# Optimization experiments

Hardware: AMD Instinct MI355X
Metric: run time of the kernel (lower is better)

Reference implementation:

```python
import jax, jax.numpy as jnp
import numpy as np

N = 50000   # nodes
E = 400000  # edges (before self-loops)
F = 128     # num_features
H = 8       # heads (layer 1)
C = 64      # hidden_channels
B = 64      # graphs in batch
K = 10      # num_classes
NEG_SLOPE = 0.2


def setup_inputs() -> dict:
    key = jax.random.key(0)
    ks = jax.random.split(key, 12)
    g = lambda k, shape, fan: jax.random.normal(k, shape, jnp.float32) / np.sqrt(fan).astype(np.float32)
    return {
        "x": jax.random.normal(ks[0], (N, F), jnp.float32),
        "edge_index": jax.random.randint(ks[1], (2, E), 0, N, jnp.int32),
        "batch": jnp.sort(jax.random.randint(ks[2], (N,), 0, B, jnp.int32)),
        "W1": g(ks[3], (F, H * C), F),
        "att_src1": g(ks[4], (H, C), C),
        "att_dst1": g(ks[5], (H, C), C),
        "b1": jnp.zeros((H * C,), jnp.float32),
        "W2": g(ks[6], (H * C, C), H * C),
        "att_src2": g(ks[7], (1, C), C),
        "att_dst2": g(ks[8], (1, C), C),
        "b2": jnp.zeros((C,), jnp.float32),
        "lin1_w": g(ks[9], (C, C), C),
        "lin1_b": jnp.zeros((C,), jnp.float32),
        "lin2_w": g(ks[10], (C, K), C),
        "lin2_b": jnp.zeros((K,), jnp.float32),
    }


def gat_conv(x, src, dst, W, att_src, att_dst, bias):
    """PyG GATConv (self-loops already appended to src/dst). x:[N,Fin] -> [N,H*C]."""
    heads, out_c = att_src.shape
    h = (x @ W).reshape(N, heads, out_c)                      # [N,H,C]
    a_s = jnp.einsum('nhc,hc->nh', h, att_src)                # [N,H]
    a_d = jnp.einsum('nhc,hc->nh', h, att_dst)
    e = jax.nn.leaky_relu(a_s[src] + a_d[dst], NEG_SLOPE)     # [E',H]
    # segment softmax over incoming edges of each destination node
    m = jax.ops.segment_max(e, dst, num_segments=N)
    e = jnp.exp(e - m[dst])
    denom = jax.ops.segment_sum(e, dst, num_segments=N)
    alpha = e / (denom[dst] + 1e-16)                          # [E',H]
    out = jax.ops.segment_sum(h[src] * alpha[:, :, None], dst, num_segments=N)  # [N,H,C]
    return out.reshape(N, heads * out_c) + bias


def reference(x, edge_index, batch, W1, att_src1, att_dst1, b1,
              W2, att_src2, att_dst2, b2, lin1_w, lin1_b, lin2_w, lin2_b):
    loops = jnp.arange(N, dtype=edge_index.dtype)
    src = jnp.concatenate([edge_index[0], loops])
    dst = jnp.concatenate([edge_index[1], loops])

    h = gat_conv(x, src, dst, W1, att_src1, att_dst1, b1)     # [N, H*C]
    h = jax.nn.elu(h)                                         # dropout inactive (eval)
    h = gat_conv(h, src, dst, W2, att_src2, att_dst2, b2)     # [N, C]
    h = jax.nn.elu(h)

    pooled = jax.ops.segment_sum(h, batch, num_segments=B)    # global_add_pool -> [B, C]
    z = jax.nn.elu(pooled @ lin1_w + lin1_b)
    logits = z @ lin2_w + lin2_b
    return jax.nn.log_softmax(logits, axis=-1)
```

## Files before the change

kernel.cpp:

```cpp
#include <hip/hip_runtime.h>
#include <hip/hip_bf16.h>

#define DEV static __device__ __forceinline__

constexpr int F1 = 128;
constexpr int H1 = 8;
constexpr int C  = 64;
constexpr int B  = 64;
constexpr int K  = 10;
constexpr float NEG = 0.2f;
constexpr unsigned SMASK = 0x07FFFFFFu;

typedef __attribute__((ext_vector_type(8))) short short8;
typedef __attribute__((ext_vector_type(4))) float floatx4;

DEV float b2f(__hip_bfloat16 x) { return __bfloat162float(x); }
DEV float elu1(float v) { return v > 0.f ? v : (__expf(v) - 1.f); }
DEV unsigned short f2bbits(float f) {
  __hip_bfloat16 b = __float2bfloat16(f);
  return *(unsigned short*)&b;
}
DEV float blo(unsigned u) { return __uint_as_float(u << 16); }
DEV float bhi(unsigned u) { return __uint_as_float(u & 0xffff0000u); }
DEV float bu(unsigned short u) { return __uint_as_float(((unsigned)u) << 16); }
DEV unsigned pack2(float lo, float hi) {
  return (unsigned)f2bbits(lo) | ((unsigned)f2bbits(hi) << 16);
}
DEV float rcp_nr(float x) {
  float r = __builtin_amdgcn_rcpf(x);
  return r * (2.f - x * r);
}


DEV int detect_dev(const void* xraw, int* lds) {
  if (threadIdx.x == 0) {
    const __hip_bfloat16* xb = (const __hip_bfloat16*)xraw;
    int bad = 0;
    for (int i = 0; i < 128; ++i) {
      float v = b2f(xb[2 * i]);
      if (!(fabsf(v) < 1e4f)) bad++;
    }
    *lds = (bad < 13) ? 1 : 0;
  }
  __syncthreads();
  return *lds;
}

#define CVT(p, i) (isbf ? b2f(((const __hip_bfloat16*)(p))[i]) : ((const float*)(p))[i])

__global__ void fused_prep_kernel(const void* x_raw, const void* w1raw,
                                  const void* as1r, const void* ad1r, const void* b1r,
                                  const void* w2raw,
                                  const void* as2r, const void* ad2r, const void* b2r,
                                  const void* l1wr, const void* l1br,
                                  const void* l2wr, const void* l2br,
                                  unsigned short* __restrict__ xbf,
                                  unsigned short* __restrict__ w1frag,
                                  unsigned short* __restrict__ w2frag,
                                  unsigned short* __restrict__ vfrag,
                                  float* __restrict__ wts,
                                  int* __restrict__ deg,
                                  float* __restrict__ pooled,
                                  int nX, int N) {
  __shared__ int fl;
  int isbf = detect_dev(x_raw, &fl);
  int gid = blockIdx.x * 256 + threadIdx.x;
  int stride = gridDim.x * 256;

  if (isbf) {
    const unsigned short* src = (const unsigned short*)x_raw;
    for (int i = gid; i < nX; i += stride) xbf[i] = src[i];
  } else {
    const float* src = (const float*)x_raw;
    for (int i = gid; i < nX; i += stride) xbf[i] = f2bbits(src[i]);
  }
  for (int i = gid; i < 512;  i += stride) {
    int hp = i >> 7, l16 = (i >> 3) & 15, nt = i & 7;
    int c = hp * 128 + nt * 16 + l16;
    wts[1024 + i] = CVT(b1r, c);
  }
  for (int i = gid; i < 64;   i += stride) wts[1536 + i] = CVT(as2r, i);
  for (int i = gid; i < 64;   i += stride) wts[1600 + i] = CVT(ad2r, i);
  for (int i = gid; i < 64;   i += stride) wts[1664 + i] = CVT(b2r, i);
  for (int i = gid; i < 4096; i += stride) wts[1728 + i] = CVT(l1wr, i);
  for (int i = gid; i < 64;   i += stride) wts[5824 + i] = CVT(l1br, i);
  for (int i = gid; i < 640;  i += stride) wts[5888 + i] = CVT(l2wr, i);
  for (int i = gid; i < 10;   i += stride) wts[6528 + i] = CVT(l2br, i);
  for (int t = gid; t < 8192; t += stride) {
    int lane = t & 63, ks = (t >> 6) & 3, nt = t >> 8;
    for (int j = 0; j < 8; ++j) {
      int k = ks * 32 + (lane >> 4) * 8 + j;
      int n = nt * 16 + (lane & 15);
      w1frag[t * 8 + j] = f2bbits(CVT(w1raw, k * 512 + n));
    }
  }
  for (int t = gid; t < 4096; t += stride) {
    int lane = t & 63, nt = (t >> 6) & 3, ks = t >> 8;
    for (int j = 0; j < 8; ++j) {
      int p = ks * 32 + (lane >> 4) * 8 + j;
      int hp = p >> 7, pl16 = (p >> 3) & 15, pnt = p & 7;
      int k = hp * 128 + pnt * 16 + pl16;
      int n = nt * 16 + (lane & 15);
      w2frag[t * 8 + j] = f2bbits(CVT(w2raw, k * 64 + n));
    }
  }
  for (int t = gid; t < 2048; t += stride) {
    int j = t & 7, lane = (t >> 3) & 63, ks = t >> 9;
    int k = ks * 32 + (lane >> 4) * 8 + j;
    int n = lane & 15;
    int hh = (n < 8) ? n : (n - 8);
    float s = 0.f;
    if (n < 8) {
      for (int c = 0; c < 64; ++c)
        s += CVT(w1raw, k * 512 + hh * 64 + c) * CVT(as1r, hh * 64 + c);
    } else {
      for (int c = 0; c < 64; ++c)
        s += CVT(w1raw, k * 512 + hh * 64 + c) * CVT(ad1r, hh * 64 + c);
    }
    vfrag[(ks * 64 + lane) * 8 + j] = f2bbits(s);
  }
  for (int i = gid; i < N; i += stride) deg[i] = 0;
  for (int i = gid; i < B * C; i += stride) pooled[i] = 0.f;
}

__global__ void deg_count_kernel(const int* __restrict__ ei, int E, int Etot,
                                 int* __restrict__ deg) {
  int e = blockIdx.x * blockDim.x + threadIdx.x;
  if (e >= Etot) return;
  int d = (e < E) ? ei[E + e] : e - E;
  atomicAdd(&deg[d], 1);
}

__global__ void scan_block_kernel(const int* __restrict__ deg,
                                  int* __restrict__ local,
                                  int* __restrict__ bsum, int N) {
  __shared__ int tmp[256];
  int t = threadIdx.x;
  int i = blockIdx.x * 256 + t;
  int v = (i < N) ? deg[i] : 0;
  tmp[t] = v;
  __syncthreads();
  for (int off = 1; off < 256; off <<= 1) {
    int u = (t >= off) ? tmp[t - off] : 0;
    __syncthreads();
    tmp[t] += u;
    __syncthreads();
  }
  if (i < N) local[i] = tmp[t] - v;
  if (t == 255) bsum[blockIdx.x] = tmp[255];
}

__global__ void scan_finish_kernel(const int* __restrict__ local,
                                   const int* __restrict__ bsum, int nb,
                                   int* __restrict__ rowptr,
                                   int* __restrict__ cursor, int N, int Etot) {
  __shared__ int tmp[256];
  __shared__ int offs;
  int t = threadIdx.x;
  int v0 = (t < nb) ? bsum[t] : 0;
  tmp[t] = v0;
  __syncthreads();
  for (int off = 1; off < 256; off <<= 1) {
    int u = (t >= off) ? tmp[t - off] : 0;
    __syncthreads();
    tmp[t] += u;
    __syncthreads();
  }
  if (t == (int)blockIdx.x) offs = tmp[t] - v0;
  __syncthreads();
  int i = blockIdx.x * 256 + t;
  if (i < N) {
    int r = local[i] + offs;
    rowptr[i] = r;
    cursor[i] = r;
  }
  if (i == 0) rowptr[N] = Etot;
}

__global__ __launch_bounds__(256) void att_scalars_kernel(
    const unsigned short* __restrict__ xbf,
    const unsigned short* __restrict__ vfrag,
    float* __restrict__ a_s, float* __restrict__ a_d,
    int N) {
  int t = threadIdx.x, w = t >> 6, lane = t & 63;
  int quad = lane >> 4, l16 = lane & 15;
  int row0 = blockIdx.x * 64 + w * 16;

  floatx4 acc = {};
  int rl = row0 + l16; if (rl >= N) rl = N - 1;
  const unsigned short* xp = xbf + (size_t)rl * 128 + quad * 8;
#pragma unroll
  for (int ks = 0; ks < 4; ++ks) {
    short8 a = *(const short8*)(xp + ks * 32);
    short8 b = *(const short8*)&vfrag[(ks * 64 + lane) * 8];
    acc = __builtin_amdgcn_mfma_f32_16x16x32_bf16(a, b, acc, 0, 0, 0);
  }
#pragma unroll
  for (int r = 0; r < 4; ++r) {
    int row = row0 + quad * 4 + r;
    if (row < N) {
      if (l16 < 8) a_s[(size_t)row * 8 + l16] = acc[r];
      else         a_d[(size_t)row * 8 + (l16 - 8)] = acc[r];
    }
  }
}

__global__ void fill_weight_kernel(const int* __restrict__ ei, int E, int Etot,
                                   const float* __restrict__ a_s,
                                   const float* __restrict__ a_d,
                                   int* __restrict__ cursor,
                                   int* __restrict__ col,
                                   unsigned short* __restrict__ wedge) {
  int e = blockIdx.x * 256 + threadIdx.x;
  if (e >= Etot) return;
  int s, d;
  if (e < E) { s = ei[e]; d = ei[E + e]; } else { s = d = e - E; }
  int pos = atomicAdd(&cursor[d], 1);
  col[pos] = s | ((d & 15) << 27);
  float4 s0 = *(const float4*)(a_s + (size_t)s * 8);
  float4 s1 = *(const float4*)(a_s + (size_t)s * 8 + 4);
  float4 d0 = *(const float4*)(a_d + (size_t)d * 8);
  float4 d1 = *(const float4*)(a_d + (size_t)d * 8 + 4);
  float v, w0, w1, w2, w3, w4, w5, w6, w7;
  v = s0.x + d0.x; v = v > 0.f ? v : NEG * v; w0 = __expf(v);
  v = s0.y + d0.y; v = v > 0.f ? v : NEG * v; w1 = __expf(v);
  v = s0.z + d0.z; v = v > 0.f ? v : NEG * v; w2 = __expf(v);
  v = s0.w + d0.w; v = v > 0.f ? v : NEG * v; w3 = __expf(v);
  v = s1.x + d1.x; v = v > 0.f ? v : NEG * v; w4 = __expf(v);
  v = s1.y + d1.y; v = v > 0.f ? v : NEG * v; w5 = __expf(v);
  v = s1.z + d1.z; v = v > 0.f ? v : NEG * v; w6 = __expf(v);
  v = s1.w + d1.w; v = v > 0.f ? v : NEG * v; w7 = __expf(v);
  uint4 o;
  o.x = pack2(w0, w1); o.y = pack2(w2, w3);
  o.z = pack2(w4, w5); o.w = pack2(w6, w7);
  *(uint4*)(wedge + (size_t)pos * 8) = o;
}

__global__ __launch_bounds__(512, 6) void aggx_gemm1_kernel(
    const unsigned short* __restrict__ xbf,
    const unsigned short* __restrict__ W1frag,
    const int* __restrict__ rowptr,
    const int* __restrict__ col,
    const unsigned short* __restrict__ wedge,
    const float* __restrict__ bias_perm,
    unsigned short* __restrict__ out1,
    int N) {
  __shared__ __align__(16) char LB[8 * 16 * 136 * 2];
  unsigned short* XgT = (unsigned short*)LB;
  unsigned short* Wm  = (unsigned short*)(LB + 8192);
  unsigned short* AggP = (unsigned short*)LB;

  int t = threadIdx.x, w = t >> 6, lane = t & 63;
  int q = lane >> 4, n = lane & 15;
  int dbase = blockIdx.x * 16;

  int R0 = rowptr[dbase];
  int R1 = rowptr[min(dbase + 16, N)];
  int nch = (R1 - R0 + 31) >> 5;

  int kp = t >> 5, pp = t & 31;
  int skey = ((pp >> 1) & 7) << 4;
  int dw = t >> 5, kw = t & 31;

  short8 onesf = {};
  if (n == 0) {
#pragma unroll
    for (int j = 0; j < 8; ++j) onesf[j] = (short)0x3F80;
  }

  floatx4 accw[8] = {};
  floatx4 accdn = {};

  for (int c = 0; c < nch; ++c) {
    int ebase = R0 + c * 32;
    __syncthreads();

    {
      int e0 = ebase + 2 * kp;
      int ec0 = (e0 < R1) ? e0 : (R1 - 1);
      int ec1 = (e0 + 1 < R1) ? (e0 + 1) : (R1 - 1);
      int s0 = col[ec0] & SMASK;
      int s1 = col[ec1] & SMASK;
      uint2 xa = *(const uint2*)(xbf + (size_t)s0 * 128 + pp * 4);
      uint2 xb = *(const uint2*)(xbf + (size_t)s1 * 128 + pp * 4);
      int base = 256 * pp + 4 * kp;
      unsigned w0 = (xa.x & 0xffffu) | (xb.x << 16);
      unsigned w1 = (xa.x >> 16) | (xb.x & 0xffff0000u);
      unsigned w2 = (xa.y & 0xffffu) | (xb.y << 16);
      unsigned w3 = (xa.y >> 16) | (xb.y & 0xffff0000u);
      *(unsigned*)((char*)XgT + ((base)       ^ skey)) = w0;
      *(unsigned*)((char*)XgT + ((base + 64)  ^ skey)) = w1;
      *(unsigned*)((char*)XgT + ((base + 128) ^ skey)) = w2;
      *(unsigned*)((char*)XgT + ((base + 192) ^ skey)) = w3;
    }
    {
      int ew = ebase + kw;
      bool evw = ew < R1;
      int ewc = evw ? ew : (R1 - 1);
      int cv = col[ewc];
      int dl = (cv >> 27) & 15;
      uint4 wv = *(const uint4*)(wedge + (size_t)ewc * 8);
      bool mine = evw && (dl == dw);
      unsigned short* wmp = Wm + dw * 32 + kw;
      wmp[0]    = mine ? (unsigned short)(wv.x & 0xffff) : 0;
      wmp[512]  = mine ? (unsigned short)(wv.x >> 16)    : 0;
      wmp[1024] = mine ? (unsigned short)(wv.y & 0xffff) : 0;
      wmp[1536] = mine ? (unsigned short)(wv.y >> 16)    : 0;
      wmp[2048] = mine ? (unsigned short)(wv.z & 0xffff) : 0;
      wmp[2560] = mine ? (unsigned short)(wv.z >> 16)    : 0;
      wmp[3072] = mine ? (unsigned short)(wv.w & 0xffff) : 0;
      wmp[3584] = mine ? (unsigned short)(wv.w >> 16)    : 0;
    }
    __syncthreads();

    short8 af = *(const short8*)(Wm + w * 512 + n * 32 + 8 * q);
    accdn = __builtin_amdgcn_mfma_f32_16x16x32_bf16(af, onesf, accdn, 0, 0, 0);
#pragma unroll
    for (int ft = 0; ft < 8; ++ft) {
      int bb = (ft * 16 + n) * 64 + 16 * q;
      bb ^= ((bb >> 9) & 7) << 4;
      short8 bfr = *(const short8*)((const char*)XgT + bb);
      accw[ft] = __builtin_amdgcn_mfma_f32_16x16x32_bf16(af, bfr, accw[ft], 0, 0, 0);
    }
  }

  __syncthreads();

  {
    float dnv[4];
#pragma unroll
    for (int r = 0; r < 4; ++r) {
      float dr = __shfl(accdn[r], lane & 48);
      dnv[r] = rcp_nr(dr + 1e-16f);
    }
#pragma unroll
    for (int ft = 0; ft < 8; ++ft)
#pragma unroll
      for (int r = 0; r < 4; ++r)
        AggP[w * 2176 + (4 * q + r) * 136 + ft * 16 + n] =
            f2bbits(accw[ft][r] * dnv[r]);
  }
  __syncthreads();

  {
    int hp = w >> 1, qq = w & 1;
    floatx4 acc2[4] = {};
    const unsigned short* Bp = W1frag + (size_t)hp * 16384;
#pragma unroll
    for (int ks = 0; ks < 4; ++ks) {
      short8 a2 = *(const short8*)&AggP[w * 2176 + n * 136 + ks * 32 + q * 8];
#pragma unroll
      for (int j = 0; j < 4; ++j) {
        int nt = qq * 4 + j;
        short8 b2 = *(const short8*)&Bp[((nt * 4 + ks) * 64 + lane) * 8];
        acc2[j] = __builtin_amdgcn_mfma_f32_16x16x32_bf16(a2, b2, acc2[j], 0, 0, 0);
      }
    }
    float4 bq = *(const float4*)&bias_perm[hp * 128 + n * 8 + qq * 4];
#pragma unroll
    for (int r = 0; r < 4; ++r) {
      int row = dbase + 4 * q + r;
      if (row < N) {
        uint2 o;
        o.x = pack2(elu1(acc2[0][r] + bq.x), elu1(acc2[1][r] + bq.y));
        o.y = pack2(elu1(acc2[2][r] + bq.z), elu1(acc2[3][r] + bq.w));
        *(uint2*)&out1[(size_t)row * 512 + hp * 128 + n * 8 + qq * 4] = o;
      }
    }
  }
}

__global__ __launch_bounds__(256) void gemm2_mfma_kernel(
    const unsigned short* __restrict__ x2bf,
    const unsigned short* __restrict__ W2frag,
    const float* __restrict__ att_src,
    const float* __restrict__ att_dst,
    unsigned short* __restrict__ h2,
    float* __restrict__ a_s, float* __restrict__ a_d,
    int N) {
  int t = threadIdx.x;
  int w = t >> 6, lane = t & 63;
  int quad = lane >> 4, l16 = lane & 15;
  int rowbase = blockIdx.x * 64 + w * 16;

  floatx4 acc[4] = {};
  int r0 = rowbase + l16; if (r0 >= N) r0 = N - 1;
  const unsigned short* p0 = x2bf + (size_t)r0 * 512 + quad * 8;
#pragma unroll
  for (int ks = 0; ks < 16; ++ks) {
    short8 a0 = *(const short8*)(p0 + ks * 32);
#pragma unroll
    for (int nt = 0; nt < 4; ++nt) {
      short8 b = *(const short8*)&W2frag[((ks * 4 + nt) * 64 + lane) * 8];
      acc[nt] = __builtin_amdgcn_mfma_f32_16x16x32_bf16(a0, b, acc[nt], 0, 0, 0);
    }
  }

  float asw[4], adw[4];
#pragma unroll
  for (int nt = 0; nt < 4; ++nt) {
    asw[nt] = att_src[nt * 16 + l16];
    adw[nt] = att_dst[nt * 16 + l16];
  }
  float ps[4] = {}, pd[4] = {};
#pragma unroll
  for (int nt = 0; nt < 4; ++nt)
#pragma unroll
    for (int r = 0; r < 4; ++r) {
      float v = acc[nt][r];
      int row = rowbase + quad * 4 + r;
      if (row < N) h2[(size_t)row * 64 + nt * 16 + l16] = f2bbits(v);
      ps[r] += v * asw[nt];
      pd[r] += v * adw[nt];
    }
#pragma unroll
  for (int r = 0; r < 4; ++r) {
    float p = ps[r], q = pd[r];
#pragma unroll
    for (int off = 1; off < 16; off <<= 1) {
      p += __shfl_xor(p, off);
      q += __shfl_xor(q, off);
    }
    int row = rowbase + quad * 4 + r;
    if (l16 == 0 && row < N) {
      a_s[row] = p;
      a_d[row] = q;
    }
  }
}

__global__ void gat_agg1_kernel(const int* __restrict__ rowptr,
                                const int* __restrict__ col,
                                const float* __restrict__ a_s,
                                const float* __restrict__ a_d,
                                const unsigned short* __restrict__ hfeat,
                                const float* __restrict__ bias,
                                unsigned short* __restrict__ out, int N) {
  int wave = threadIdx.x >> 6, lane = threadIdx.x & 63;
  int d = blockIdx.x * 4 + wave;
  if (d >= N) return;
  int beg = rowptr[d], end = rowptr[d + 1];
  int qg = lane >> 4, l16 = lane & 15;
  float adv = a_d[d];
  const uint2* hfu = (const uint2*)hfeat;
  float acc[4] = {};
  float wsum = 0.f;
#pragma unroll 2
  for (int i = beg + qg; i < end; i += 4) {
    int s = col[i] & SMASK;
    float v = a_s[s] + adv;
    v = v > 0.f ? v : NEG * v;
    float wv = __expf(v);
    wsum += wv;
    uint2 u = hfu[(size_t)s * 16 + l16];
    acc[0] += wv * blo(u.x); acc[1] += wv * bhi(u.x);
    acc[2] += wv * blo(u.y); acc[3] += wv * bhi(u.y);
  }
#pragma unroll
  for (int off = 16; off <= 32; off <<= 1) {
#pragma unroll
    for (int j = 0; j < 4; ++j) acc[j] += __shfl_xor(acc[j], off);
    wsum += __shfl_xor(wsum, off);
  }
  float winv = 1.f / (wsum + 1e-16f);
  float4 bb = ((const float4*)bias)[l16];
  float r0 = elu1(acc[0] * winv + bb.x), r1 = elu1(acc[1] * winv + bb.y);
  float r2 = elu1(acc[2] * winv + bb.z), r3 = elu1(acc[3] * winv + bb.w);
  if (qg == 0) {
    uint2 o; o.x = pack2(r0, r1); o.y = pack2(r2, r3);
    ((uint2*)out)[(size_t)d * 16 + l16] = o;
  }
}

__global__ void pool_kernel(const unsigned short* __restrict__ out2,
                            const int* __restrict__ batch,
                            float* __restrict__ pooled, int N) {
  int wave = threadIdx.x >> 6, lane = threadIdx.x & 63;
  int seg = blockIdx.x * 4 + wave;
  int start = seg * 16;
  if (start >= N) return;
  int end = min(start + 16, N);
  int cur = batch[start];
  float acc = 0.f;
  for (int n = start; n < end; ++n) {
    int bn = batch[n];
    if (bn != cur) {
      unsafeAtomicAdd(&pooled[cur * 64 + lane], acc);
      acc = 0.f; cur = bn;
    }
    acc += bu(out2[(size_t)n * 64 + lane]);
  }
  unsafeAtomicAdd(&pooled[cur * 64 + lane], acc);
}

__global__ void head_kernel(const float* __restrict__ pooled,
                            const float* __restrict__ lin1_w,
                            const float* __restrict__ lin1_b,
                            const float* __restrict__ lin2_w,
                            const float* __restrict__ lin2_b,
                            const void* __restrict__ x_raw,
                            void* __restrict__ outv) {
  __shared__ float P[C];
  __shared__ float Zs[C];
  __shared__ float Ls[K];
  __shared__ float lse_s;
  __shared__ int fl;
  int isbf = detect_dev(x_raw, &fl);
  int g = blockIdx.x, t = threadIdx.x;
  P[t] = pooled[g * C + t];
  __syncthreads();
  float acc = lin1_b[t];
  for (int k = 0; k < C; ++k) acc += P[k] * lin1_w[k * C + t];
  Zs[t] = elu1(acc);
  __syncthreads();
  if (t < K) {
    float a = lin2_b[t];
    for (int k = 0; k < C; ++k) a += Zs[k] * lin2_w[k * K + t];
    Ls[t] = a;
  }
  __syncthreads();
  if (t == 0) {
    float mx = -1e30f;
    for (int c = 0; c < K; ++c) mx = fmaxf(mx, Ls[c]);
    float s = 0.f;
    for (int c = 0; c < K; ++c) s += __expf(Ls[c] - mx);
    lse_s = mx + __logf(s);
  }
  __syncthreads();
  if (t < K) {
    float val = Ls[t] - lse_s;
    if (isbf) ((__hip_bfloat16*)outv)[g * K + t] = __float2bfloat16(val);
    else      ((float*)outv)[g * K + t] = val;
  }
}

extern "C" void kernel_launch(void* const* d_in, const int* in_sizes, int n_in,
                              void* d_out, int out_size, void* d_ws, size_t ws_size,
                              hipStream_t stream) {
  const void* x_raw = d_in[0];
  const int*  ei    = (const int*)d_in[1];
  const int*  batch = (const int*)d_in[2];

  const int N    = in_sizes[2];
  const int E    = in_sizes[1] / 2;
  const int Etot = E + N;
  const int nb   = (N + 255) / 256;

  float* ws   = (float*)d_ws;
  size_t off  = 0;

  float* wts = ws + off; off += 6544;
  float* b1w  = wts + 1024;
  float* as2w = wts + 1536;
  float* ad2w = wts + 1600;
  float* b2w  = wts + 1664;
  float* l1w  = wts + 1728;
  float* l1b  = wts + 5824;
  float* l2w  = wts + 5888;
  float* l2b  = wts + 6528;

  unsigned short* xbf    = (unsigned short*)(ws + off); off += (size_t)N * 64;
  unsigned short* w1frag = (unsigned short*)(ws + off); off += 32768;
  unsigned short* w2frag = (unsigned short*)(ws + off); off += 16384;
  unsigned short* vfrag  = (unsigned short*)(ws + off); off += 1024;
  unsigned short* wedge  = (unsigned short*)(ws + off); off += (size_t)Etot * 4;
  unsigned short* out1bf = (unsigned short*)(ws + off); off += (size_t)N * 256;
  unsigned short* h2bf   = (unsigned short*)(ws + off); off += (size_t)N * 32;
  unsigned short* out2bf = (unsigned short*)(ws + off); off += (size_t)N * 32;
  float* as1  = ws + off; off += (size_t)N * H1;
  float* ad1  = ws + off; off += (size_t)N * H1;
  float* as2  = ws + off; off += (size_t)N;
  float* ad2  = ws + off; off += (size_t)N;
  float* pooled = ws + off; off += (size_t)B * C;

  int* ibase  = (int*)(ws + off);
  int* deg    = ibase;                 ibase += N;
  int* cursor = ibase;                 ibase += N;
  int* rowptr = ibase;                 ibase += N + 1;
  int* locals = ibase;                 ibase += N;
  int* bsum   = ibase;                 ibase += 256;
  int* col    = ibase;                 ibase += Etot;

  fused_prep_kernel<<<1024, 256, 0, stream>>>(
      x_raw, d_in[3], d_in[4], d_in[5], d_in[6], d_in[7], d_in[8], d_in[9],
      d_in[10], d_in[11], d_in[12], d_in[13], d_in[14],
      xbf, w1frag, w2frag, vfrag, wts, deg, pooled, in_sizes[0], N);

  deg_count_kernel<<<(Etot + 255) / 256, 256, 0, stream>>>(ei, E, Etot, deg);
  scan_block_kernel<<<nb, 256, 0, stream>>>(deg, locals, bsum, N);
  scan_finish_kernel<<<nb, 256, 0, stream>>>(locals, bsum, nb, rowptr, cursor, N, Etot);

  att_scalars_kernel<<<(N + 63) / 64, 256, 0, stream>>>(xbf, vfrag, as1, ad1, N);

  fill_weight_kernel<<<(Etot + 255) / 256, 256, 0, stream>>>(
      ei, E, Etot, as1, ad1, cursor, col, wedge);

  aggx_gemm1_kernel<<<(N + 15) / 16, 512, 0, stream>>>(
      xbf, w1frag, rowptr, col, wedge, b1w, out1bf, N);

  gemm2_mfma_kernel<<<(N + 63) / 64, 256, 0, stream>>>(out1bf, w2frag, as2w, ad2w,
                                                       h2bf, as2, ad2, N);
  gat_agg1_kernel<<<(N + 3) / 4, 256, 0, stream>>>(rowptr, col, as2, ad2, h2bf, b2w, out2bf, N);

  pool_kernel<<<(N + 63) / 64, 256, 0, stream>>>(out2bf, batch, pooled, N);
  head_kernel<<<B, 64, 0, stream>>>(pooled, l1w, l1b, l2w, l2b, x_raw, (void*)d_out);
}
```

Baseline: 296.0 us.

## Double-buffer LDS and prefetch next edge chunk gathers in aggregation GEMM kernel

Restructures the edge-chunk loop of the layer-1 aggregation kernel into a register-prefetch plus LDS double-buffer pipeline. The gathers for chunk c+1 are issued before the MFMA work on chunk c, and one of the two barriers per iteration is removed. The XOR swizzle key is also changed to match the new layout. Together these aim to hide gather latency and cut synchronisation, at the cost of extra registers and twice the LDS footprint, which may lower occupancy under the 512x6 launch bounds.

```diff
diff --git a/kernel.cpp b/kernel.cpp
--- a/kernel.cpp
+++ b/kernel.cpp
@@ -246,8 +246,6 @@
     unsigned short* __restrict__ out1,
     int N) {
   __shared__ __align__(16) char LB[8 * 16 * 136 * 2];
-  unsigned short* XgT = (unsigned short*)LB;
-  unsigned short* Wm  = (unsigned short*)(LB + 8192);
   unsigned short* AggP = (unsigned short*)LB;
 
   int t = threadIdx.x, w = t >> 6, lane = t & 63;
@@ -259,7 +257,7 @@
   int nch = (R1 - R0 + 31) >> 5;
 
   int kp = t >> 5, pp = t & 31;
-  int skey = ((pp >> 1) & 7) << 4;
+  int skey = (pp & 7) << 4;
   int dw = t >> 5, kw = t & 31;
 
   short8 onesf = {};
@@ -271,55 +269,72 @@
   floatx4 accw[8] = {};
   floatx4 accdn = {};
 
+  uint2 pxa, pxb;
+  uint4 pwv;
+  int pcv;
+  {
+    int e0 = R0 + 2 * kp;
+    int ec0 = min(e0, R1 - 1), ec1 = min(e0 + 1, R1 - 1);
+    int s0 = col[ec0] & SMASK;
+    int s1 = col[ec1] & SMASK;
+    pxa = *(const uint2*)(xbf + (size_t)s0 * 128 + pp * 4);
+    pxb = *(const uint2*)(xbf + (size_t)s1 * 128 + pp * 4);
+    int ew = min(R0 + kw, R1 - 1);
+    pcv = col[ew];
+    pwv = *(const uint4*)(wedge + (size_t)ew * 8);
+  }
+
   for (int c = 0; c < nch; ++c) {
-    int ebase = R0 + c * 32;
-    __syncthreads();
+    char* Lb = LB + (c & 1) * 16384;
+    unsigned short* XgTc = (unsigned short*)Lb;
+    unsigned short* Wmc  = (unsigned short*)(Lb + 8192);
 
     {
+      int base = 256 * pp + 4 * kp;
+      unsigned w0 = (pxa.x & 0xffffu) | (pxb.x << 16);
+      unsigned w1 = (pxa.x >> 16) | (pxb.x & 0xffff0000u);
+      unsigned w2 = (pxa.y & 0xffffu) | (pxb.y << 16);
+      unsigned w3 = (pxa.y >> 16) | (pxb.y & 0xffff0000u);
+      *(unsigned*)(Lb + ((base)       ^ skey)) = w0;
+      *(unsigned*)(Lb + ((base + 64)  ^ skey)) = w1;
+      *(unsigned*)(Lb + ((base + 128) ^ skey)) = w2;
+      *(unsigned*)(Lb + ((base + 192) ^ skey)) = w3;
+
+      int ew = R0 + c * 32 + kw;
+      int dl = (pcv >> 27) & 15;
+      bool mine = (ew < R1) && (dl == dw);
+      unsigned short* wmp = Wmc + dw * 32 + kw;
+      wmp[0]    = mine ? (unsigned short)(pwv.x & 0xffff) : 0;
+      wmp[512]  = mine ? (unsigned short)(pwv.x >> 16)    : 0;
+      wmp[1024] = mine ? (unsigned short)(pwv.y & 0xffff) : 0;
+      wmp[1536] = mine ? (unsigned short)(pwv.y >> 16)    : 0;
+      wmp[2048] = mine ? (unsigned short)(pwv.z & 0xffff) : 0;
+      wmp[2560] = mine ? (unsigned short)(pwv.z >> 16)    : 0;
+      wmp[3072] = mine ? (unsigned short)(pwv.w & 0xffff) : 0;
+      wmp[3584] = mine ? (unsigned short)(pwv.w >> 16)    : 0;
+    }
+    if (c + 1 < nch) {
+      int ebase = R0 + (c + 1) * 32;
       int e0 = ebase + 2 * kp;
-      int ec0 = (e0 < R1) ? e0 : (R1 - 1);
-      int ec1 = (e0 + 1 < R1) ? (e0 + 1) : (R1 - 1);
+      int ec0 = min(e0, R1 - 1), ec1 = min(e0 + 1, R1 - 1);
       int s0 = col[ec0] & SMASK;
       int s1 = col[ec1] & SMASK;
-      uint2 xa = *(const uint2*)(xbf + (size_t)s0 * 128 + pp * 4);
-      uint2 xb = *(const uint2*)(xbf + (size_t)s1 * 128 + pp * 4);
-      int base = 256 * pp + 4 * kp;
-      unsigned w0 = (xa.x & 0xffffu) | (xb.x << 16);
-      unsigned w1 = (xa.x >> 16) | (xb.x & 0xffff0000u);
-      unsigned w2 = (xa.y & 0xffffu) | (xb.y << 16);
-      unsigned w3 = (xa.y >> 16) | (xb.y & 0xffff0000u);
-      *(unsigned*)((char*)XgT + ((base)       ^ skey)) = w0;
-      *(unsigned*)((char*)XgT + ((base + 64)  ^ skey)) = w1;
-      *(unsigned*)((char*)XgT + ((base + 128) ^ skey)) = w2;
-      *(unsigned*)((char*)XgT + ((base + 192) ^ skey)) = w3;
-    }
-    {
-      int ew = ebase + kw;
-      bool evw = ew < R1;
-      int ewc = evw ? ew : (R1 - 1);
-      int cv = col[ewc];
-      int dl = (cv >> 27) & 15;
-      uint4 wv = *(const uint4*)(wedge + (size_t)ewc * 8);
-      bool mine = evw && (dl == dw);
-      unsigned short* wmp = Wm + dw * 32 + kw;
-      wmp[0]    = mine ? (unsigned short)(wv.x & 0xffff) : 0;
-      wmp[512]  = mine ? (unsigned short)(wv.x >> 16)    : 0;
-      wmp[1024] = mine ? (unsigned short)(wv.y & 0xffff) : 0;
-      wmp[1536] = mine ? (unsigned short)(wv.y >> 16)    : 0;
-      wmp[2048] = mine ? (unsigned short)(wv.z & 0xffff) : 0;
-      wmp[2560] = mine ? (unsigned short)(wv.z >> 16)    : 0;
-      wmp[3072] = mine ? (unsigned short)(wv.w & 0xffff) : 0;
-      wmp[3584] = mine ? (unsigned short)(wv.w >> 16)    : 0;
+      pxa = *(const uint2*)(xbf + (size_t)s0 * 128 + pp * 4);
+      pxb = *(const uint2*)(xbf + (size_t)s1 * 128 + pp * 4);
+      int ew = min(ebase + kw, R1 - 1);
+      pcv = col[ew];
+      pwv = *(const uint4*)(wedge + (size_t)ew * 8);
     }
     __syncthreads();
 
-    short8 af = *(const short8*)(Wm + w * 512 + n * 32 + 8 * q);
+    short8 af = *(const short8*)(Wmc + w * 512 + n * 32 + 8 * q);
     accdn = __builtin_amdgcn_mfma_f32_16x16x32_bf16(af, onesf, accdn, 0, 0, 0);
 #pragma unroll
     for (int ft = 0; ft < 8; ++ft) {
-      int bb = (ft * 16 + n) * 64 + 16 * q;
-      bb ^= ((bb >> 9) & 7) << 4;
-      short8 bfr = *(const short8*)((const char*)XgT + bb);
+      int f = ft * 16 + n;
+      int bb = f * 64 + 16 * q;
+      bb ^= ((f >> 2) & 7) << 4;
+      short8 bfr = *(const short8*)((const char*)XgTc + bb);
       accw[ft] = __builtin_amdgcn_mfma_f32_16x16x32_bf16(af, bfr, accw[ft], 0, 0, 0);
     }
   }
```

New measurement: 285.6 us. 3.5% less time.
